# Kernel optimization log

Hardware: AMD Instinct MI355X
Metric: run time of the kernel (lower is better)

The kernel has to match this reference:

```python
import jax, jax.numpy as jnp
import numpy as np

N_NODES = 100000
N_EDGES = 3200000
NFEAT, HID, NCLASS = 256, 32, 16


def setup_inputs() -> dict:
    key = jax.random.key(0)
    ks = jax.random.split(key, 6)
    x = jax.random.normal(ks[0], (N_NODES, NFEAT), dtype=jnp.float32)
    edge_index = jax.random.randint(ks[1], (2, N_EDGES), 0, N_NODES, dtype=jnp.int64)
    edge_weight = jax.random.uniform(ks[2], (N_EDGES,), dtype=jnp.float32)
    # Glorot-ish init for the two GCNConv linear weights; bias zeros (PyG default init zeros bias)
    W1 = jax.random.normal(ks[3], (NFEAT, HID), dtype=jnp.float32) * (1.0 / np.sqrt(NFEAT))
    b1 = jnp.zeros((HID,), dtype=jnp.float32)
    W2 = jax.random.normal(ks[4], (HID, NCLASS), dtype=jnp.float32) * (1.0 / np.sqrt(HID))
    b2 = jnp.zeros((NCLASS,), dtype=jnp.float32)
    return {"x": x, "edge_index": edge_index, "edge_weight": edge_weight,
            "W1": W1, "b1": b1, "W2": W2, "b2": b2}


def _gcn_norm(row, col, w, n):
    """PyG gcn_norm: add self-loops (weight 1), symmetric normalization."""
    loop = jnp.arange(n, dtype=row.dtype)
    row = jnp.concatenate([row, loop])
    col = jnp.concatenate([col, loop])
    w = jnp.concatenate([w, jnp.ones((n,), dtype=w.dtype)])
    deg = jax.ops.segment_sum(w, col, num_segments=n)  # degree at target nodes
    dinv = jnp.where(deg > 0, jax.lax.rsqrt(deg), 0.0)
    norm = dinv[row] * w * dinv[col]
    return row, col, norm


def _gcn_conv(x, W, b, row, col, norm, n):
    xw = x @ W                                  # [N, out]
    msg = xw[row] * norm[:, None]               # gather at source + scale
    out = jax.ops.segment_sum(msg, col, num_segments=n)  # scatter-add at target
    return out + b


def reference(x, edge_index, edge_weight, W1, b1, W2, b2):
    n = x.shape[0]
    row, col, norm = _gcn_norm(edge_index[0], edge_index[1], edge_weight, n)
    h = jax.nn.relu(_gcn_conv(x, W1, b1, row, col, norm, n))
    # dropout is identity in eval mode
    logits = _gcn_conv(h, W2, b2, row, col, norm, n)
    return jax.nn.log_softmax(logits, axis=1)
```

## Files before the change

kernel.cpp:

```cpp
#include <hip/hip_runtime.h>

#define N_NODES 100000
#define N_EDGES 3200000
#define NFEAT 256
#define HID 32
#define NCLASS 16

#define NB 64
#define CHUNK (N_EDGES / NB)
#define RN2 32768
#define NR2 ((N_NODES + RN2 - 1) / RN2)

#define SCAN_TPB 256
#define SCAN_EPB 1024
#define SCAN_NBLK ((N_NODES + SCAN_EPB - 1) / SCAN_EPB)

#define XPAD 133

__device__ inline unsigned short f2bf(float f) {
    unsigned u = __float_as_uint(f);
    u += 0x7FFFu + ((u >> 16) & 1u);
    return (unsigned short)(u >> 16);
}
__device__ inline float bf2f(unsigned short s) {
    return __uint_as_float((unsigned)s << 16);
}
__device__ inline void bf8_unpack(uint4 g, float* f) {
    f[0] = __uint_as_float(g.x << 16); f[1] = __uint_as_float(g.x & 0xFFFF0000u);
    f[2] = __uint_as_float(g.y << 16); f[3] = __uint_as_float(g.y & 0xFFFF0000u);
    f[4] = __uint_as_float(g.z << 16); f[5] = __uint_as_float(g.z & 0xFFFF0000u);
    f[6] = __uint_as_float(g.w << 16); f[7] = __uint_as_float(g.w & 0xFFFF0000u);
}

__global__ __launch_bounds__(1024) void k_count(const int* __restrict__ col,
                                                unsigned* __restrict__ H,
                                                unsigned short* __restrict__ pos) {
    __shared__ unsigned hist[RN2 / 2];
    int t = threadIdx.x, b = blockIdx.x, r = blockIdx.y;
    int base = r * RN2;
    const int* cc = col + (size_t)b * CHUNK;
    unsigned short* pp = pos + (size_t)b * CHUNK;
    for (int i = t; i < RN2 / 2; i += 1024) hist[i] = 0;
    __syncthreads();
    for (int i = t; i < CHUNK; i += 1024) {
        unsigned d = (unsigned)cc[i] - (unsigned)base;
        if (d < RN2) {
            unsigned old = atomicAdd(&hist[d >> 1], 1u << ((d & 1) * 16));
            pp[i] = (unsigned short)((old >> ((d & 1) * 16)) & 0xFFFFu);
        }
    }
    __syncthreads();
    int lim = min(RN2, N_NODES - base);
    unsigned* Hb = H + (size_t)b * N_NODES;
    for (int i = t; i < lim; i += 1024)
        Hb[base + i] = (hist[i >> 1] >> ((i & 1) * 16)) & 0xFFFFu;
}

__global__ void k_rowsum(const unsigned* __restrict__ H, int* __restrict__ cnt) {
    int n = blockIdx.x * 256 + threadIdx.x;
    if (n >= N_NODES) return;
    unsigned s = 0;
    #pragma unroll 8
    for (int b = 0; b < NB; ++b) s += H[(size_t)b * N_NODES + n];
    cnt[n] = (int)s;
}

__global__ __launch_bounds__(SCAN_TPB) void k_scanA(const int* __restrict__ cnt,
                                                    int* __restrict__ offs,
                                                    int* __restrict__ bsum) {
    __shared__ int s[SCAN_TPB];
    int t = threadIdx.x;
    int base = blockIdx.x * SCAN_EPB + t * 4;
    int v0 = (base + 0 < N_NODES) ? cnt[base + 0] : 0;
    int v1 = (base + 1 < N_NODES) ? cnt[base + 1] : 0;
    int v2 = (base + 2 < N_NODES) ? cnt[base + 2] : 0;
    int v3 = (base + 3 < N_NODES) ? cnt[base + 3] : 0;
    int sum = v0 + v1 + v2 + v3;
    s[t] = sum;
    __syncthreads();
    for (int off = 1; off < SCAN_TPB; off <<= 1) {
        int x = (t >= off) ? s[t - off] : 0;
        __syncthreads();
        s[t] += x;
        __syncthreads();
    }
    int excl = s[t] - sum;
    if (t == SCAN_TPB - 1) bsum[blockIdx.x] = s[t];
    int run = excl;
    if (base + 0 < N_NODES) offs[base + 0] = run; run += v0;
    if (base + 1 < N_NODES) offs[base + 1] = run; run += v1;
    if (base + 2 < N_NODES) offs[base + 2] = run; run += v2;
    if (base + 3 < N_NODES) offs[base + 3] = run;
}

__global__ __launch_bounds__(128) void k_scanB(int* __restrict__ bsum) {
    __shared__ int s[128];
    int t = threadIdx.x;
    int v = (t < SCAN_NBLK) ? bsum[t] : 0;
    s[t] = v;
    __syncthreads();
    for (int off = 1; off < 128; off <<= 1) {
        int x = (t >= off) ? s[t - off] : 0;
        __syncthreads();
        s[t] += x;
        __syncthreads();
    }
    if (t < SCAN_NBLK) bsum[t] = s[t] - v;
}

__global__ __launch_bounds__(SCAN_TPB) void k_scanC(int* __restrict__ offs,
                                                    const int* __restrict__ bsum) {
    int t = threadIdx.x;
    int add = bsum[blockIdx.x];
    int base = blockIdx.x * SCAN_EPB + t * 4;
    #pragma unroll
    for (int i = 0; i < 4; ++i) {
        int idx = base + i;
        if (idx < N_NODES) offs[idx] += add;
    }
    if (blockIdx.x == 0 && t == 0) offs[N_NODES] = N_EDGES;
}

__global__ void k_bprefix(unsigned* __restrict__ H, const int* __restrict__ offs) {
    int n = blockIdx.x * 256 + threadIdx.x;
    if (n >= N_NODES) return;
    unsigned run = (unsigned)offs[n];
    for (int b = 0; b < NB; ++b) {
        size_t idx = (size_t)b * N_NODES + n;
        unsigned v = H[idx];
        H[idx] = run;
        run += v;
    }
}

__global__ void k_emit(const int* __restrict__ row, const int* __restrict__ col,
                       const float* __restrict__ w, const unsigned* __restrict__ B,
                       const unsigned short* __restrict__ pos,
                       float2* __restrict__ ein) {
    int e = blockIdx.x * 256 + threadIdx.x;
    if (e >= N_EDGES) return;
    int b = e / CHUNK;
    int c = col[e];
    unsigned p = B[(size_t)b * N_NODES + c] + (unsigned)pos[e];
    ein[p] = make_float2(__int_as_float(row[e]), w[e]);
}

__global__ void k_deg(const float2* __restrict__ ein, const int* __restrict__ offs,
                      float* __restrict__ dinv) {
    int idx = blockIdx.x * 256 + threadIdx.x;
    int n = idx >> 2, l = idx & 3;
    if (n >= N_NODES) return;
    int s = offs[n], e = offs[n + 1];
    float sum = 0.f;
    for (int p = s + l; p < e; p += 4) sum += ein[p].y;
    sum += __shfl_xor(sum, 1, 4);
    sum += __shfl_xor(sum, 2, 4);
    if (l == 0) dinv[n] = rsqrtf(1.0f + sum);
}

__global__ __launch_bounds__(256) void k_gemm1s(const float* __restrict__ x,
                                                const float* __restrict__ W1,
                                                unsigned short* __restrict__ xwp) {
    __shared__ float sWc[32 * HID];
    __shared__ float sX[32 * XPAD];
    int t = threadIdx.x;
    long rowbase = (long)blockIdx.x * 128;
    int kbase = blockIdx.y * 128;
    unsigned short* xw = xwp + (size_t)blockIdx.y * N_NODES * HID;
    int tr = t >> 3;
    int tc = t & 7;
    float acc[4][4] = {};
    for (int k0 = kbase; k0 < kbase + 128; k0 += 32) {
        *(float4*)&sWc[t * 4] = *(const float4*)&W1[k0 * HID + t * 4];
        #pragma unroll
        for (int p = 0; p < 4; ++p) {
            int rt = (t >> 3) + p * 32;
            int kk = (t & 7) * 4;
            long grow = rowbase + rt;
            float4 v = make_float4(0.f, 0.f, 0.f, 0.f);
            if (grow < N_NODES) v = *(const float4*)&x[grow * NFEAT + k0 + kk];
            sX[(kk + 0) * XPAD + rt] = v.x; sX[(kk + 1) * XPAD + rt] = v.y;
            sX[(kk + 2) * XPAD + rt] = v.z; sX[(kk + 3) * XPAD + rt] = v.w;
        }
        __syncthreads();
        #pragma unroll 8
        for (int kk = 0; kk < 32; ++kk) {
            float xv[4], wv[4];
            xv[0] = sX[kk * XPAD + tr * 4 + 0];
            xv[1] = sX[kk * XPAD + tr * 4 + 1];
            xv[2] = sX[kk * XPAD + tr * 4 + 2];
            xv[3] = sX[kk * XPAD + tr * 4 + 3];
            *(float4*)&wv[0] = *(float4*)&sWc[kk * HID + tc * 4];
            #pragma unroll
            for (int m = 0; m < 4; ++m)
                #pragma unroll
                for (int n = 0; n < 4; ++n)
                    acc[m][n] = fmaf(xv[m], wv[n], acc[m][n]);
        }
        __syncthreads();
    }
    #pragma unroll
    for (int m = 0; m < 4; ++m) {
        long r = rowbase + tr * 4 + m;
        if (r < N_NODES) {
            ushort4 o;
            o.x = f2bf(acc[m][0]); o.y = f2bf(acc[m][1]);
            o.z = f2bf(acc[m][2]); o.w = f2bf(acc[m][3]);
            *(ushort4*)&xw[r * HID + tc * 4] = o;
        }
    }
}

__global__ void k_comb(const unsigned short* __restrict__ xwp,
                       ushort4* __restrict__ xwb) {
    int i = blockIdx.x * 256 + threadIdx.x;
    const ushort4* p0 = (const ushort4*)xwp;
    const ushort4* p1 = p0 + 800000;
    ushort4 a = p0[i], b = p1[i];
    ushort4 o;
    o.x = f2bf(bf2f(a.x) + bf2f(b.x));
    o.y = f2bf(bf2f(a.y) + bf2f(b.y));
    o.z = f2bf(bf2f(a.z) + bf2f(b.z));
    o.w = f2bf(bf2f(a.w) + bf2f(b.w));
    xwb[i] = o;
}

__global__ __launch_bounds__(256) void k_gather1(const unsigned short* __restrict__ xwb,
                                                 const float* __restrict__ dinv,
                                                 const float2* __restrict__ ein,
                                                 const int* __restrict__ offs,
                                                 const float* __restrict__ b1,
                                                 float* __restrict__ h) {
    int idx = blockIdx.x * 256 + threadIdx.x;
    int n = idx >> 3, l = idx & 7;
    int c4 = l * 4;
    const ushort4* xb = (const ushort4*)xwb;
    float di = dinv[n];
    ushort4 q = xb[(long)n * 8 + l];
    float4 acc = make_float4(bf2f(q.x) * di, bf2f(q.y) * di,
                             bf2f(q.z) * di, bf2f(q.w) * di);
    int s = offs[n], e = offs[n + 1];
    for (int p0 = s; p0 < e; p0 += 8) {
        int pl = p0 + l;
        float2 pr = (pl < e) ? ein[pl] : make_float2(__int_as_float(n), 0.f);
        int ri = __float_as_int(pr.x);
        pr.y *= dinv[ri];
        #pragma unroll
        for (int j = 0; j < 8; ++j) {
            int r = __shfl(ri, j, 8);
            float nm = __shfl(pr.y, j, 8);
            ushort4 g = xb[(long)r * 8 + l];
            acc.x = fmaf(bf2f(g.x), nm, acc.x);
            acc.y = fmaf(bf2f(g.y), nm, acc.y);
            acc.z = fmaf(bf2f(g.z), nm, acc.z);
            acc.w = fmaf(bf2f(g.w), nm, acc.w);
        }
    }
    float4 bb = *(const float4*)&b1[c4];
    acc.x = fmaxf(fmaf(acc.x, di, bb.x), 0.f);
    acc.y = fmaxf(fmaf(acc.y, di, bb.y), 0.f);
    acc.z = fmaxf(fmaf(acc.z, di, bb.z), 0.f);
    acc.w = fmaxf(fmaf(acc.w, di, bb.w), 0.f);
    *(float4*)&h[(long)n * HID + c4] = acc;
}

__global__ __launch_bounds__(256) void k_gemm2(const float* __restrict__ h,
                                               const float* __restrict__ W2,
                                               unsigned short* __restrict__ hwb) {
    __shared__ float sH[64][33];
    __shared__ float sW2[HID * NCLASS];
    int t = threadIdx.x;
    if (t < 128) {
        int idx = t * 4;
        *(float4*)&sW2[idx] = *(const float4*)&W2[idx];
    }
    long base = (long)blockIdx.x * 64;
    #pragma unroll
    for (int i = 0; i < 2; ++i) {
        int idx = t + i * 256;
        int rt = idx >> 3, kk = (idx & 7) * 4;
        long gr = base + rt;
        float4 v = make_float4(0.f, 0.f, 0.f, 0.f);
        if (gr < N_NODES) v = *(const float4*)&h[gr * HID + kk];
        sH[rt][kk + 0] = v.x; sH[rt][kk + 1] = v.y;
        sH[rt][kk + 2] = v.z; sH[rt][kk + 3] = v.w;
    }
    __syncthreads();
    int r = t >> 2, c4 = (t & 3) * 4;
    float acc[4] = {};
    #pragma unroll
    for (int k = 0; k < HID; ++k) {
        float hv = sH[r][k];
        float wv[4];
        *(float4*)&wv[0] = *(float4*)&sW2[k * NCLASS + c4];
        #pragma unroll
        for (int n = 0; n < 4; ++n) acc[n] = fmaf(hv, wv[n], acc[n]);
    }
    long gr = base + r;
    if (gr < N_NODES) {
        ushort4 o;
        o.x = f2bf(acc[0]); o.y = f2bf(acc[1]);
        o.z = f2bf(acc[2]); o.w = f2bf(acc[3]);
        *(ushort4*)&hwb[gr * NCLASS + c4] = o;
    }
}

__global__ __launch_bounds__(256) void k_gather2(const unsigned short* __restrict__ hwb,
                                                 const float* __restrict__ dinv,
                                                 const float2* __restrict__ ein,
                                                 const int* __restrict__ offs,
                                                 const float* __restrict__ b2,
                                                 float* __restrict__ out) {
    int idx = blockIdx.x * 256 + threadIdx.x;
    int n = idx >> 1, l = idx & 1;
    if (n >= N_NODES) return;
    int c8 = l * 8;
    const uint4* hb = (const uint4*)hwb;
    float di = dinv[n];
    float acc[8], f[8];
    bf8_unpack(hb[(long)n * 2 + l], f);
    #pragma unroll
    for (int k = 0; k < 8; ++k) acc[k] = f[k] * di;
    int s = offs[n], e = offs[n + 1];
    for (int p0 = s; p0 < e; p0 += 8) {
        float2 pr[4];
        int rr[4];
        #pragma unroll
        for (int k = 0; k < 4; ++k) {
            int pl = p0 + k * 2 + l;
            pr[k] = (pl < e) ? ein[pl] : make_float2(__int_as_float(n), 0.f);
            rr[k] = __float_as_int(pr[k].x);
            pr[k].y *= dinv[rr[k]];
        }
        #pragma unroll
        for (int k = 0; k < 4; ++k) {
            #pragma unroll
            for (int j = 0; j < 2; ++j) {
                int r = __shfl(rr[k], j, 2);
                float nm = __shfl(pr[k].y, j, 2);
                bf8_unpack(hb[(long)r * 2 + l], f);
                #pragma unroll
                for (int q = 0; q < 8; ++q) acc[q] = fmaf(f[q], nm, acc[q]);
            }
        }
    }
    float4 bb0 = *(const float4*)&b2[c8];
    float4 bb1 = *(const float4*)&b2[c8 + 4];
    float v[8];
    v[0] = fmaf(acc[0], di, bb0.x); v[1] = fmaf(acc[1], di, bb0.y);
    v[2] = fmaf(acc[2], di, bb0.z); v[3] = fmaf(acc[3], di, bb0.w);
    v[4] = fmaf(acc[4], di, bb1.x); v[5] = fmaf(acc[5], di, bb1.y);
    v[6] = fmaf(acc[6], di, bb1.z); v[7] = fmaf(acc[7], di, bb1.w);
    float m = v[0];
    #pragma unroll
    for (int k = 1; k < 8; ++k) m = fmaxf(m, v[k]);
    m = fmaxf(m, __shfl_xor(m, 1, 2));
    float sum = 0.f;
    #pragma unroll
    for (int k = 0; k < 8; ++k) sum += __expf(v[k] - m);
    sum += __shfl_xor(sum, 1, 2);
    float ls = m + __logf(sum);
    float4 o0 = make_float4(v[0] - ls, v[1] - ls, v[2] - ls, v[3] - ls);
    float4 o1 = make_float4(v[4] - ls, v[5] - ls, v[6] - ls, v[7] - ls);
    *(float4*)&out[(long)n * NCLASS + c8] = o0;
    *(float4*)&out[(long)n * NCLASS + c8 + 4] = o1;
}

extern "C" void kernel_launch(void* const* d_in, const int* in_sizes, int n_in,
                              void* d_out, int out_size, void* d_ws, size_t ws_size,
                              hipStream_t stream) {
    const float* x  = (const float*)d_in[0];
    const int*   ei = (const int*)d_in[1];
    const float* w  = (const float*)d_in[2];
    const float* W1 = (const float*)d_in[3];
    const float* b1 = (const float*)d_in[4];
    const float* W2 = (const float*)d_in[5];
    const float* b2 = (const float*)d_in[6];
    float* out = (float*)d_out;

    const int* row = ei;
    const int* col = ei + N_EDGES;

    float* ws = (float*)d_ws;
    float2* ein = (float2*)ws;
    unsigned* H = (unsigned*)(ws + 2 * (size_t)N_EDGES);
    unsigned short* pos = (unsigned short*)(ws + 2 * (size_t)N_EDGES + (size_t)NB * N_NODES);
    float* h = (float*)pos;
    float* dinv = ws + 2 * (size_t)N_EDGES + (size_t)NB * N_NODES + N_EDGES;
    int* cnt = (int*)(dinv + N_NODES);
    int* offs = cnt + N_NODES;
    int* bsum = offs + N_NODES + 1;
    size_t xwp_off = (size_t)(2 * (size_t)N_EDGES + (size_t)NB * N_NODES + N_EDGES
                              + 3 * N_NODES + 1 + 128);
    xwp_off = (xwp_off + 3) & ~(size_t)3;
    unsigned short* xwp = (unsigned short*)(ws + xwp_off);
    unsigned short* xwb = (unsigned short*)(ws + xwp_off + 3200000);
    unsigned short* hwb = xwb + (size_t)N_NODES * HID;

    const int B = 256;

    k_count<<<dim3(NB, NR2), 1024, 0, stream>>>(col, H, pos);
    k_rowsum<<<(N_NODES + B - 1) / B, B, 0, stream>>>(H, cnt);
    k_scanA<<<SCAN_NBLK, SCAN_TPB, 0, stream>>>(cnt, offs, bsum);
    k_scanB<<<1, 128, 0, stream>>>(bsum);
    k_scanC<<<SCAN_NBLK, SCAN_TPB, 0, stream>>>(offs, bsum);
    k_bprefix<<<(N_NODES + B - 1) / B, B, 0, stream>>>(H, offs);
    k_emit<<<(N_EDGES + B - 1) / B, B, 0, stream>>>(row, col, w, H, pos, ein);

    k_deg<<<(N_NODES * 4 + B - 1) / B, B, 0, stream>>>(ein, offs, dinv);

    k_gemm1s<<<dim3((N_NODES + 127) / 128, 2), 256, 0, stream>>>(x, W1, xwp);
    k_comb<<<(N_NODES * HID / 4) / B, B, 0, stream>>>(xwp, (ushort4*)xwb);
    k_gather1<<<(N_NODES * 8) / B, B, 0, stream>>>(xwb, dinv, ein, offs, b1, h);

    k_gemm2<<<(N_NODES + 63) / 64, B, 0, stream>>>(h, W2, hwb);
    k_gather2<<<(N_NODES * 2 + B - 1) / B, B, 0, stream>>>(hwb, dinv, ein, offs, b2, out);
}
```

Before: 284.4 us.

## Fuse bucket prefix into rowsum as 16-bit table, XCD-aware emit mapping

Merges the per-bucket prefix computation into the row-sum pass, storing a 16-bit per-bucket local prefix instead of rewriting the 32-bit histogram with global offsets. This removes the separate k_bprefix pass and halves the size of the table the emit kernel gathers from. The emit kernel now adds offs[c] itself and remaps block IDs so that each XCD handles a fixed set of edge chunks, aiming for better L2 locality on the per-chunk prefix rows. The cost is an extra offs gather per edge and reliance on per-node counts fitting in 16 bits.

```diff
diff --git a/kernel.cpp b/kernel.cpp
--- a/kernel.cpp
+++ b/kernel.cpp
@@ -10,6 +10,7 @@
 #define CHUNK (N_EDGES / NB)
 #define RN2 32768
 #define NR2 ((N_NODES + RN2 - 1) / RN2)
+#define BPC 196
 
 #define SCAN_TPB 256
 #define SCAN_EPB 1024
@@ -56,13 +57,19 @@
         Hb[base + i] = (hist[i >> 1] >> ((i & 1) * 16)) & 0xFFFFu;
 }
 
-__global__ void k_rowsum(const unsigned* __restrict__ H, int* __restrict__ cnt) {
+__global__ void k_prefix16(const unsigned* __restrict__ H,
+                           unsigned short* __restrict__ SP, int* __restrict__ cnt) {
     int n = blockIdx.x * 256 + threadIdx.x;
     if (n >= N_NODES) return;
-    unsigned s = 0;
+    unsigned run = 0;
     #pragma unroll 8
-    for (int b = 0; b < NB; ++b) s += H[(size_t)b * N_NODES + n];
-    cnt[n] = (int)s;
+    for (int b = 0; b < NB; ++b) {
+        size_t i = (size_t)b * N_NODES + n;
+        unsigned v = H[i];
+        SP[i] = (unsigned short)run;
+        run += v;
+    }
+    cnt[n] = (int)run;
 }
 
 __global__ __launch_bounds__(SCAN_TPB) void k_scanA(const int* __restrict__ cnt,
@@ -121,27 +128,25 @@
     if (blockIdx.x == 0 && t == 0) offs[N_NODES] = N_EDGES;
 }
 
-__global__ void k_bprefix(unsigned* __restrict__ H, const int* __restrict__ offs) {
-    int n = blockIdx.x * 256 + threadIdx.x;
-    if (n >= N_NODES) return;
-    unsigned run = (unsigned)offs[n];
-    for (int b = 0; b < NB; ++b) {
-        size_t idx = (size_t)b * N_NODES + n;
-        unsigned v = H[idx];
-        H[idx] = run;
-        run += v;
-    }
-}
-
-__global__ void k_emit(const int* __restrict__ row, const int* __restrict__ col,
-                       const float* __restrict__ w, const unsigned* __restrict__ B,
-                       const unsigned short* __restrict__ pos,
-                       float2* __restrict__ ein) {
-    int e = blockIdx.x * 256 + threadIdx.x;
-    if (e >= N_EDGES) return;
-    int b = e / CHUNK;
+__global__ __launch_bounds__(256) void k_emit(const int* __restrict__ row,
+                                              const int* __restrict__ col,
+                                              const float* __restrict__ w,
+                                              const int* __restrict__ offs,
+                                              const unsigned short* __restrict__ SP,
+                                              const unsigned short* __restrict__ pos,
+                                              float2* __restrict__ ein) {
+    int bid = blockIdx.x;
+    int xcd = bid & 7;
+    int q = bid >> 3;
+    int m = q / BPC;
+    int j = q - m * BPC;
+    int b = xcd + 8 * m;
+    int i0 = j * 256 + threadIdx.x;
+    if (i0 >= CHUNK) return;
+    size_t e = (size_t)b * CHUNK + i0;
     int c = col[e];
-    unsigned p = B[(size_t)b * N_NODES + c] + (unsigned)pos[e];
+    unsigned p = (unsigned)offs[c] + (unsigned)SP[(size_t)b * N_NODES + c]
+               + (unsigned)pos[e];
     ein[p] = make_float2(__int_as_float(row[e]), w[e]);
 }
 
@@ -396,16 +401,16 @@
     unsigned short* xwp = (unsigned short*)(ws + xwp_off);
     unsigned short* xwb = (unsigned short*)(ws + xwp_off + 3200000);
     unsigned short* hwb = xwb + (size_t)N_NODES * HID;
+    unsigned short* SP = hwb + (size_t)N_NODES * NCLASS;
 
     const int B = 256;
 
     k_count<<<dim3(NB, NR2), 1024, 0, stream>>>(col, H, pos);
-    k_rowsum<<<(N_NODES + B - 1) / B, B, 0, stream>>>(H, cnt);
+    k_prefix16<<<(N_NODES + B - 1) / B, B, 0, stream>>>(H, SP, cnt);
     k_scanA<<<SCAN_NBLK, SCAN_TPB, 0, stream>>>(cnt, offs, bsum);
     k_scanB<<<1, 128, 0, stream>>>(bsum);
     k_scanC<<<SCAN_NBLK, SCAN_TPB, 0, stream>>>(offs, bsum);
-    k_bprefix<<<(N_NODES + B - 1) / B, B, 0, stream>>>(H, offs);
-    k_emit<<<(N_EDGES + B - 1) / B, B, 0, stream>>>(row, col, w, H, pos, ein);
+    k_emit<<<8 * 8 * BPC, B, 0, stream>>>(row, col, w, offs, SP, pos, ein);
 
     k_deg<<<(N_NODES * 4 + B - 1) / B, B, 0, stream>>>(ein, offs, dinv);
 
```

After: 263.5 us (median of 2 runs). 1.08x faster.
